# Kernel optimization log

Hardware: AMD Instinct MI355X
Metric: run time of the kernel (lower is better)

Reference implementation:

```python
import jax, jax.numpy as jnp
import numpy as np

N = 50000
E = 800000

def sage_conv(x, src, dst, Wl, Wr, b):
    # PyG SAGEConv (mean aggr): out = lin_l(mean_{j in N(i)} x_j) + lin_r(x_i)
    ones = jnp.ones((src.shape[0],), x.dtype)
    deg = jax.ops.segment_sum(ones, dst, num_segments=N)          # [N]
    agg = jax.ops.segment_sum(x[src], dst, num_segments=N)        # [N, d]
    agg = agg / jnp.maximum(deg, 1.0)[:, None]                    # mean, 0 for isolated nodes
    return agg @ Wl + x @ Wr + b


def setup_inputs() -> dict:
    key = jax.random.key(0)
    ks = jax.random.split(key, 12)
    d_in, d_hid, d_mid, d_out = 128, 128, 256, 64
    sc = lambda d: 1.0 / np.sqrt(d)
    inp = {
        "x0": jax.random.normal(ks[0], (N, d_in), jnp.float32),
        "x1": jax.random.normal(ks[1], (N, d_in), jnp.float32),
        "edge_index": jax.random.randint(ks[2], (2, E), 0, N, dtype=jnp.int64),
        "Wl0": jax.random.normal(ks[3], (d_in, d_hid), jnp.float32) * sc(d_in),
        "Wr0": jax.random.normal(ks[4], (d_in, d_hid), jnp.float32) * sc(d_in),
        "b0": jnp.zeros((d_hid,), jnp.float32),
        "Wl1": jax.random.normal(ks[5], (d_in, d_hid), jnp.float32) * sc(d_in),
        "Wr1": jax.random.normal(ks[6], (d_in, d_hid), jnp.float32) * sc(d_in),
        "b1": jnp.zeros((d_hid,), jnp.float32),
        "Wlm": jax.random.normal(ks[7], (d_mid, d_mid), jnp.float32) * sc(d_mid),
        "Wrm": jax.random.normal(ks[8], (d_mid, d_mid), jnp.float32) * sc(d_mid),
        "bm": jnp.zeros((d_mid,), jnp.float32),
        "Wlo": jax.random.normal(ks[9], (d_mid, d_out), jnp.float32) * sc(d_mid),
        "Wro": jax.random.normal(ks[10], (d_mid, d_out), jnp.float32) * sc(d_mid),
        "bo": jnp.zeros((d_out,), jnp.float32),
    }
    return inp


def reference(x0, x1, edge_index, Wl0, Wr0, b0, Wl1, Wr1, b1, Wlm, Wrm, bm, Wlo, Wro, bo):
    src, dst = edge_index[0], edge_index[1]
    # initial branch convs + relu (dropout is identity in eval mode)
    h0 = jax.nn.relu(sage_conv(x0, src, dst, Wl0, Wr0, b0))
    h1 = jax.nn.relu(sage_conv(x1, src, dst, Wl1, Wr1, b1))
    h = jnp.concatenate([h0, h1], axis=-1)                        # [N, 256]
    # middle conv(s)
    h = jax.nn.relu(sage_conv(h, src, dst, Wlm, Wrm, bm))
    # final conv, no activation
    return sage_conv(h, src, dst, Wlo, Wro, bo)                   # [N, 64]
```

## Files before the change

kernel.cpp:

```cpp
#include <hip/hip_runtime.h>
#include <cstdint>
#include <cstddef>


typedef __attribute__((ext_vector_type(8))) short short8;
typedef __attribute__((ext_vector_type(4))) float f32x4;

#define CAPLOG 6
#define CAP 64
#define BSH 7
#define MAXBUK 512
#define BCAP 2560
#define EPB 4096

__device__ __forceinline__ ushort f2bf(float f) {
    unsigned u = __float_as_uint(f);
    u += 0x7fffu + ((u >> 16) & 1u);
    return (ushort)(u >> 16);
}
__device__ __forceinline__ float bf2f(ushort u) {
    return __uint_as_float((unsigned)u << 16);
}

__global__ void prep_kernel(
    int eb, int xb, int E, int N, int nbuk,
    const int* __restrict__ src, const int* __restrict__ dst,
    int* __restrict__ gcursor, unsigned* __restrict__ binned,
    const float* x0, const float* x1, ushort* xc,
    const float* __restrict__ Wl0, const float* __restrict__ Wr0,
    const float* __restrict__ Wl1, const float* __restrict__ Wr1,
    const float* __restrict__ Wlm, const float* __restrict__ Wrm,
    const float* __restrict__ Wlo, const float* __restrict__ Wro,
    const float* __restrict__ b0, const float* __restrict__ b1,
    ushort* __restrict__ Wcat1, ushort* __restrict__ Wcat2,
    ushort* __restrict__ Wcat3, float* __restrict__ bcat01) {
    __shared__ int hist[MAXBUK];
    int tid = threadIdx.x;
    if (blockIdx.x < eb) {
        for (int b = tid; b < MAXBUK; b += 256) hist[b] = 0;
        __syncthreads();
        int base = blockIdx.x * EPB;
        unsigned ep[16];
        unsigned rk[16];
#pragma unroll
        for (int j = 0; j < 16; ++j) {
            int i = base + j * 256 + tid;
            rk[j] = 0xFFFFFFFFu;
            if (i < E) {
                int s = src[i], d = dst[i];
                int b = d >> BSH;
                int r = atomicAdd(&hist[b], 1);
                ep[j] = ((unsigned)(d & ((1 << BSH) - 1)) << 16) | (unsigned)s;
                rk[j] = ((unsigned)b << 16) | (unsigned)r;
            }
        }
        __syncthreads();
        for (int b = tid; b < nbuk; b += 256) {
            int c = hist[b];
            hist[b] = c ? atomicAdd(&gcursor[b], c) : 0;
        }
        __syncthreads();
#pragma unroll
        for (int j = 0; j < 16; ++j) {
            if (rk[j] == 0xFFFFFFFFu) continue;
            int b = rk[j] >> 16;
            int pos = hist[b] + (int)(rk[j] & 0xFFFFu);
            if (pos < BCAP) binned[(size_t)b * BCAP + pos] = ep[j];
        }
        return;
    }
    if (blockIdx.x < eb + xb) {
        int gid = (blockIdx.x - eb) * blockDim.x + tid;
        int w = gid >> 5, lane = gid & 31;
        if (w >= N) return;
        float4 a = *((const float4*)(x0 + (size_t)w * 128) + lane);
        float4 b = *((const float4*)(x1 + (size_t)w * 128) + lane);
        ushort4 ua; ua.x = f2bf(a.x); ua.y = f2bf(a.y);
        ua.z = f2bf(a.z); ua.w = f2bf(a.w);
        ushort4 ub; ub.x = f2bf(b.x); ub.y = f2bf(b.y);
        ub.z = f2bf(b.z); ub.w = f2bf(b.w);
        *((ushort4*)(xc + (size_t)w * 256) + lane) = ua;
        *((ushort4*)(xc + (size_t)w * 256 + 128) + lane) = ub;
        return;
    }
    int idx = (blockIdx.x - eb - xb) * blockDim.x + tid;
    if (idx < 65536) {
        int n = idx >> 8, k = idx & 255;
        int half = n >> 7, nl = n & 127;
        const float* Wl = half ? Wl1 : Wl0;
        const float* Wr = half ? Wr1 : Wr0;
        float v = (k < 128) ? Wl[(size_t)k * 128 + nl]
                            : Wr[(size_t)(k - 128) * 128 + nl];
        Wcat1[idx] = f2bf(v);
    } else if (idx < 65536 + 131072) {
        int i2 = idx - 65536;
        int n = i2 >> 9, k = i2 & 511;
        float v = (k < 256) ? Wlm[(size_t)k * 256 + n]
                            : Wrm[(size_t)(k - 256) * 256 + n];
        Wcat2[i2] = f2bf(v);
    } else if (idx < 65536 + 131072 + 32768) {
        int i3 = idx - (65536 + 131072);
        int n = i3 >> 8, k = i3 & 255;
        float v = (n < 64) ? Wlo[(size_t)k * 64 + n]
                           : Wro[(size_t)k * 64 + (n - 64)];
        Wcat3[i3] = f2bf(v);
    } else if (idx < 65536 + 131072 + 32768 + 256) {
        int i4 = idx - (65536 + 131072 + 32768);
        bcat01[i4] = (i4 < 128) ? b0[i4] : b1[i4 - 128];
    }
}

__global__ void bin2col_kernel(const unsigned* __restrict__ binned,
                               const int* __restrict__ gcursor,
                               ushort* __restrict__ col,
                               int* __restrict__ deg, int N) {
    __shared__ int h2[1 << BSH];
    int tid = threadIdx.x;
    int b = blockIdx.x;
    if (tid < (1 << BSH)) h2[tid] = 0;
    __syncthreads();
    int cnt = min(gcursor[b], BCAP);
    for (int i = tid; i < cnt; i += 256) {
        unsigned e = binned[(size_t)b * BCAP + i];
        int ld = e >> 16;
        int r = atomicAdd(&h2[ld], 1);
        if (r < CAP)
            col[(((size_t)((b << BSH) + ld)) << CAPLOG) + r] = (ushort)(e & 0xFFFFu);
    }
    __syncthreads();
    if (tid < (1 << BSH)) {
        int d = (b << BSH) + tid;
        if (d < N) deg[d] = h2[tid];
    }
}

__device__ __forceinline__ int wave_sort64(int v, int lane) {
#pragma unroll
    for (int k = 2; k <= 64; k <<= 1) {
#pragma unroll
        for (int j = k >> 1; j > 0; j >>= 1) {
            int other = __shfl_xor(v, j, 64);
            bool takeMax = (((lane & j) != 0) == ((lane & k) == 0));
            v = takeMax ? max(v, other) : min(v, other);
        }
    }
    return v;
}


template <int SORT>
__global__ void agg_bf16_kernel(const ushort* __restrict__ src,
                                const int* __restrict__ deg,
                                ushort* __restrict__ col,
                                ushort* __restrict__ outt, int N) {
    int gid = blockIdx.x * blockDim.x + threadIdx.x;
    int w = gid >> 6, lane = gid & 63;
    if (w >= N) return;
    int len = min(deg[w], CAP);
    int beg = w << CAPLOG;
    int colv = (lane < len) ? (int)col[beg + lane] : 0x7fffffff;
    if (SORT) {
        colv = wave_sort64(colv, lane);
        if (lane < len) col[beg + lane] = (ushort)colv;
    }
    float s0 = 0.f, s1 = 0.f, s2 = 0.f, s3 = 0.f;
    int k = 0;
    for (; k + 8 <= len; k += 8) {
        ushort4 v[8];
#pragma unroll
        for (int j = 0; j < 8; ++j) {
            int r = __builtin_amdgcn_readlane(colv, k + j);
            v[j] = *((const ushort4*)(src + (size_t)r * 256) + lane);
        }
#pragma unroll
        for (int j = 0; j < 8; ++j) {
            s0 += bf2f(v[j].x); s1 += bf2f(v[j].y);
            s2 += bf2f(v[j].z); s3 += bf2f(v[j].w);
        }
    }
    if (k + 4 <= len) {
        ushort4 v[4];
#pragma unroll
        for (int j = 0; j < 4; ++j) {
            int r = __builtin_amdgcn_readlane(colv, k + j);
            v[j] = *((const ushort4*)(src + (size_t)r * 256) + lane);
        }
#pragma unroll
        for (int j = 0; j < 4; ++j) {
            s0 += bf2f(v[j].x); s1 += bf2f(v[j].y);
            s2 += bf2f(v[j].z); s3 += bf2f(v[j].w);
        }
        k += 4;
    }
    for (; k < len; ++k) {
        int r = __builtin_amdgcn_readlane(colv, k);
        ushort4 v = *((const ushort4*)(src + (size_t)r * 256) + lane);
        s0 += bf2f(v.x); s1 += bf2f(v.y); s2 += bf2f(v.z); s3 += bf2f(v.w);
    }
    float inv = 1.0f / (float)max(len, 1);
    ushort4 o;
    o.x = f2bf(s0 * inv); o.y = f2bf(s1 * inv);
    o.z = f2bf(s2 * inv); o.w = f2bf(s3 * inv);
    *((ushort4*)(outt + (size_t)w * 256) + lane) = o;
}


__global__ void agg64_add_kernel(const ushort* __restrict__ Z,
                                 const int* __restrict__ deg,
                                 const ushort* __restrict__ col,
                                 float* __restrict__ out, int N) {
    int gid = blockIdx.x * blockDim.x + threadIdx.x;
    int w = gid >> 6, lane = gid & 63;
    if (w >= N) return;
    int len = min(deg[w], CAP);
    int beg = w << CAPLOG;
    int colv = (lane < len) ? (int)col[beg + lane] : 0;
    float s = 0.f;
    int k = 0;
    for (; k + 8 <= len; k += 8) {
        float t0 = 0.f, t1 = 0.f, t2 = 0.f, t3 = 0.f;
#pragma unroll
        for (int j = 0; j < 8; j += 4) {
            int r0 = __builtin_amdgcn_readlane(colv, k + j);
            int r1 = __builtin_amdgcn_readlane(colv, k + j + 1);
            int r2 = __builtin_amdgcn_readlane(colv, k + j + 2);
            int r3 = __builtin_amdgcn_readlane(colv, k + j + 3);
            t0 += bf2f(Z[(size_t)r0 * 64 + lane]);
            t1 += bf2f(Z[(size_t)r1 * 64 + lane]);
            t2 += bf2f(Z[(size_t)r2 * 64 + lane]);
            t3 += bf2f(Z[(size_t)r3 * 64 + lane]);
        }
        s += (t0 + t1) + (t2 + t3);
    }
    if (k + 4 <= len) {
        int r0 = __builtin_amdgcn_readlane(colv, k);
        int r1 = __builtin_amdgcn_readlane(colv, k + 1);
        int r2 = __builtin_amdgcn_readlane(colv, k + 2);
        int r3 = __builtin_amdgcn_readlane(colv, k + 3);
        float t0 = bf2f(Z[(size_t)r0 * 64 + lane]);
        float t1 = bf2f(Z[(size_t)r1 * 64 + lane]);
        float t2 = bf2f(Z[(size_t)r2 * 64 + lane]);
        float t3 = bf2f(Z[(size_t)r3 * 64 + lane]);
        s += (t0 + t1) + (t2 + t3);
        k += 4;
    }
    for (; k < len; ++k) {
        int r = __builtin_amdgcn_readlane(colv, k);
        s += bf2f(Z[(size_t)r * 64 + lane]);
    }
    float inv = 1.0f / (float)max(len, 1);
    out[(size_t)w * 64 + lane] += s * inv;
}

template <int K1, int K2, int MODE>
__global__ __launch_bounds__(256) void rs2_gemm_kernel(
    const ushort* __restrict__ A1, const ushort* __restrict__ A2, int lda,
    const ushort* __restrict__ Wg, const float* __restrict__ bias,
    ushort* __restrict__ D, float* __restrict__ D2, int M) {
    constexpr int KTOT = K1 + K2;
    constexpr int NCHUNK = KTOT / 128;
    constexpr int PK = 136;
    __shared__ __align__(16) ushort Bs[128 * PK];

    int y = blockIdx.y;
    if (MODE == 0) { A1 += y * 128; A2 += y * 128; }
    if (MODE != 2) {
        Wg += (size_t)y * 128 * KTOT;
        bias += y * 128;
        D += y * 128;
    }

    int tid = threadIdx.x;
    int m0 = blockIdx.x * 128;
    int wave = tid >> 6, lane = tid & 63;
    int lr = lane & 15, lq = lane >> 4;

    int mrow[2];
#pragma unroll
    for (int mt = 0; mt < 2; ++mt)
        mrow[mt] = min(m0 + wave * 32 + mt * 16 + lr, M - 1);

    f32x4 acc[2][8];
#pragma unroll
    for (int i = 0; i < 2; ++i)
#pragma unroll
        for (int j = 0; j < 8; ++j) acc[i][j] = (f32x4){0.f, 0.f, 0.f, 0.f};

    auto loadA = [&](int kp, short8* a) {
#pragma unroll
        for (int mt = 0; mt < 2; ++mt) {
            const ushort* srcp = (K2 == 0 || kp < K1)
                                     ? (A1 + (size_t)mrow[mt] * lda + kp)
                                     : (A2 + (size_t)mrow[mt] * lda + (kp - K1));
            a[mt] = *(const short8*)(srcp + lq * 8);
        }
    };

    short8 acur[2], anx[2];
    loadA(0, acur);

#pragma unroll
    for (int kc = 0; kc < NCHUNK; ++kc) {
        if (kc) __syncthreads();
#pragma unroll
        for (int i = 0; i < 8; ++i) {
            int e = (tid + i * 256) * 8;
            int row = e >> 7, colc = e & 127;
            float4 v = *(const float4*)(Wg + (size_t)row * KTOT + kc * 128 + colc);
            *(float4*)&Bs[row * PK + colc] = v;
        }
        __syncthreads();

#pragma unroll
        for (int ks = 0; ks < 4; ++ks) {
            int kpn = kc * 128 + (ks + 1) * 32;
            if (kpn < KTOT) loadA(kpn, anx);
            short8 b[8];
#pragma unroll
            for (int nt = 0; nt < 8; ++nt)
                b[nt] = *(const short8*)&Bs[(nt * 16 + lr) * PK + ks * 32 + lq * 8];
#pragma unroll
            for (int nt = 0; nt < 8; ++nt) {
                acc[0][nt] = __builtin_amdgcn_mfma_f32_16x16x32_bf16(
                    acur[0], b[nt], acc[0][nt], 0, 0, 0);
                acc[1][nt] = __builtin_amdgcn_mfma_f32_16x16x32_bf16(
                    acur[1], b[nt], acc[1][nt], 0, 0, 0);
            }
            acur[0] = anx[0];
            acur[1] = anx[1];
        }
    }

#pragma unroll
    for (int nt = 0; nt < 8; ++nt) {
        int c = nt * 16 + lr;
#pragma unroll
        for (int mt = 0; mt < 2; ++mt) {
#pragma unroll
            for (int r = 0; r < 4; ++r) {
                int m = m0 + wave * 32 + mt * 16 + lq * 4 + r;
                if (m >= M) continue;
                float v = acc[mt][nt][r];
                if (MODE == 2) {
                    if (c < 64) D[(size_t)m * 64 + c] = f2bf(v);
                    else        D2[(size_t)m * 64 + (c - 64)] = v + bias[c - 64];
                } else {
                    v = fmaxf(v + bias[c], 0.f);
                    D[(size_t)m * 256 + c] = f2bf(v);
                }
            }
        }
    }
}


extern "C" void kernel_launch(void* const* d_in, const int* in_sizes, int n_in,
                              void* d_out, int out_size, void* d_ws, size_t ws_size,
                              hipStream_t stream) {
    const float* x0 = (const float*)d_in[0];
    const float* x1 = (const float*)d_in[1];
    const int* ei = (const int*)d_in[2];
    const float* Wl0 = (const float*)d_in[3];
    const float* Wr0 = (const float*)d_in[4];
    const float* b0 = (const float*)d_in[5];
    const float* Wl1 = (const float*)d_in[6];
    const float* Wr1 = (const float*)d_in[7];
    const float* b1 = (const float*)d_in[8];
    const float* Wlm = (const float*)d_in[9];
    const float* Wrm = (const float*)d_in[10];
    const float* bm = (const float*)d_in[11];
    const float* Wlo = (const float*)d_in[12];
    const float* Wro = (const float*)d_in[13];
    const float* bo = (const float*)d_in[14];

    const int N = in_sizes[0] / 128;
    const int E = in_sizes[2] / 2;
    const int* srcI = ei;
    const int* dstI = ei + E;

    ushort* xc  = (ushort*)d_in[0];
    ushort* hb  = (ushort*)d_in[1];
    ushort* hmb = (ushort*)d_in[0];
    float* out = (float*)d_out;

    const int nbuk = (N + (1 << BSH) - 1) >> BSH;

    char* ws = (char*)d_ws;
    size_t used = 0;
    auto carve = [&](size_t bytes) {
        char* p = ws + used;
        used += (bytes + 63) & ~(size_t)63;
        return p;
    };
    int* deg = (int*)carve((size_t)N * 4);
    ushort* col = (ushort*)carve((size_t)N * CAP * 2);
    ushort* aggb = (ushort*)carve((size_t)N * 256 * 2);
    ushort* Zb   = (ushort*)carve((size_t)N * 64 * 2);
    unsigned* binned = (unsigned*)carve((size_t)nbuk * BCAP * 4);
    int* gcursor = (int*)carve((size_t)nbuk * 4);
    ushort* Wcat1 = (ushort*)carve(256 * 256 * 2);
    ushort* Wcat2 = (ushort*)carve(256 * 512 * 2);
    ushort* Wcat3 = (ushort*)carve(128 * 256 * 2);
    float* bcat01 = (float*)carve(256 * 4);
    if (used > ws_size) return;

    const int eb = (E + EPB - 1) / EPB;
    const int xb = (N * 32 + 255) / 256;
    const int ab = (N * 64 + 255) / 256;
    const int wb = (229632 + 255) / 256;
    const int gb = (N + 127) / 128;
    const ushort* UN = nullptr;

    hipMemsetAsync(gcursor, 0, (size_t)nbuk * 4, stream);
    prep_kernel<<<eb + xb + wb, 256, 0, stream>>>(
        eb, xb, E, N, nbuk, srcI, dstI, gcursor, binned, x0, x1, xc,
        Wl0, Wr0, Wl1, Wr1, Wlm, Wrm, Wlo, Wro, b0, b1,
        Wcat1, Wcat2, Wcat3, bcat01);
    bin2col_kernel<<<nbuk, 256, 0, stream>>>(binned, gcursor, col, deg, N);

    agg_bf16_kernel<1><<<ab, 256, 0, stream>>>(xc, deg, col, aggb, N);
    rs2_gemm_kernel<128, 128, 0><<<dim3(gb, 2), 256, 0, stream>>>(
        aggb, xc, 256, Wcat1, bcat01, hb, nullptr, N);

    agg_bf16_kernel<0><<<ab, 256, 0, stream>>>(hb, deg, col, aggb, N);
    rs2_gemm_kernel<256, 256, 1><<<dim3(gb, 2), 256, 0, stream>>>(
        aggb, hb, 256, Wcat2, bm, hmb, nullptr, N);

    rs2_gemm_kernel<256, 0, 2><<<dim3(gb, 1), 256, 0, stream>>>(
        hmb, UN, 256, Wcat3, bo, Zb, out, N);
    agg64_add_kernel<<<ab, 256, 0, stream>>>(Zb, deg, col, out, N);
}
```

Before: 363.7 us.

## Add register-resident A, full-N-width GEMM kernel for middle SAGE layer

Replaces the middle-layer GEMM (K=512, N=256) with a new kernel in which each block computes 64 rows by all 256 output columns. Each wave keeps its 16-row A fragment in registers, streamed directly from global memory with a one-step prefetch, while the weight tile is staged in padded shared memory per 64-wide K chunk. This avoids splitting N across two grid columns, which reread A, and avoids staging A in LDS. In exchange it uses 64 accumulator registers per lane, re-reads the full weight matrix per block, and issues narrow uncoalesced A loads.

New measurement: 397.9 us. 1.09x slower.

```diff
diff --git a/kernel.cpp b/kernel.cpp
--- a/kernel.cpp
+++ b/kernel.cpp
@@ -353,6 +353,73 @@
     }
 }
 
+__global__ __launch_bounds__(256) void rs3_gemm_kernel(
+    const ushort* __restrict__ A1, const ushort* __restrict__ A2,
+    const ushort* __restrict__ Wg, const float* __restrict__ bias,
+    ushort* __restrict__ D, int M) {
+    constexpr int KTOT = 512;
+    constexpr int PK = 72;
+    __shared__ __align__(16) ushort Bs[256 * PK];
+
+    int tid = threadIdx.x;
+    int m0 = blockIdx.x * 64;
+    int wave = tid >> 6, lane = tid & 63;
+    int lr = lane & 15, lq = lane >> 4;
+
+    int mrow = min(m0 + wave * 16 + lr, M - 1);
+
+    f32x4 acc[16];
+#pragma unroll
+    for (int j = 0; j < 16; ++j) acc[j] = (f32x4){0.f, 0.f, 0.f, 0.f};
+
+    auto loadA = [&](int kp, short8* a) {
+        const ushort* srcp = (kp < 256) ? (A1 + (size_t)mrow * 256 + kp)
+                                        : (A2 + (size_t)mrow * 256 + (kp - 256));
+        *a = *(const short8*)(srcp + lq * 8);
+    };
+
+    short8 acur, anx;
+    loadA(0, &acur);
+
+#pragma unroll
+    for (int kc = 0; kc < KTOT / 64; ++kc) {
+        if (kc) __syncthreads();
+#pragma unroll
+        for (int i = 0; i < 8; ++i) {
+            int e = (tid + i * 256) * 8;
+            int row = e >> 6, colc = e & 63;
+            float4 v = *(const float4*)(Wg + (size_t)row * KTOT + kc * 64 + colc);
+            *(float4*)&Bs[row * PK + colc] = v;
+        }
+        __syncthreads();
+
+#pragma unroll
+        for (int ks = 0; ks < 2; ++ks) {
+            int kpn = kc * 64 + (ks + 1) * 32;
+            if (kpn < KTOT) loadA(kpn, &anx);
+#pragma unroll
+            for (int nt = 0; nt < 16; ++nt) {
+                short8 b = *(const short8*)&Bs[(nt * 16 + lr) * PK + ks * 32 + lq * 8];
+                acc[nt] = __builtin_amdgcn_mfma_f32_16x16x32_bf16(
+                    acur, b, acc[nt], 0, 0, 0);
+            }
+            acur = anx;
+        }
+    }
+
+#pragma unroll
+    for (int nt = 0; nt < 16; ++nt) {
+        int c = nt * 16 + lr;
+#pragma unroll
+        for (int r = 0; r < 4; ++r) {
+            int m = m0 + wave * 16 + lq * 4 + r;
+            if (m >= M) continue;
+            float v = fmaxf(acc[nt][r] + bias[c], 0.f);
+            D[(size_t)m * 256 + c] = f2bf(v);
+        }
+    }
+}
+
 
 extern "C" void kernel_launch(void* const* d_in, const int* in_sizes, int n_in,
                               void* d_out, int out_size, void* d_ws, size_t ws_size,
@@ -409,6 +476,7 @@
     const int ab = (N * 64 + 255) / 256;
     const int wb = (229632 + 255) / 256;
     const int gb = (N + 127) / 128;
+    const int g3 = (N + 63) / 64;
     const ushort* UN = nullptr;
 
     hipMemsetAsync(gcursor, 0, (size_t)nbuk * 4, stream);
@@ -423,8 +491,7 @@
         aggb, xc, 256, Wcat1, bcat01, hb, nullptr, N);
 
     agg_bf16_kernel<0><<<ab, 256, 0, stream>>>(hb, deg, col, aggb, N);
-    rs2_gemm_kernel<256, 256, 1><<<dim3(gb, 2), 256, 0, stream>>>(
-        aggb, hb, 256, Wcat2, bm, hmb, nullptr, N);
+    rs3_gemm_kernel<<<g3, 256, 0, stream>>>(aggb, hb, Wcat2, bm, hmb, N);
 
     rs2_gemm_kernel<256, 0, 2><<<dim3(gb, 1), 256, 0, stream>>>(
         hmb, UN, 256, Wcat3, bo, Zb, out, N);
```
